# Kernel optimization log

Hardware: AMD Instinct MI355X
Metric: run time of the kernel (lower is better)

## Reference

```python
import jax, jax.numpy as jnp
import numpy as np

# dims: batch, d_features(m), n_subsets, sub_size(k=ceil(m/n)), heads, d_k, d_v, conv kernel, d_out
B, M, N, K, H, DK, DV, KER, D = 512, 4096, 64, 64, 8, 32, 4, 3, 4096
DOUT_PER = D // N  # d_out_per_subset = 64
EPS_LN = 1e-5      # torch nn.LayerNorm default eps


def setup_inputs() -> dict:
    key = jax.random.key(0)
    ks = jax.random.split(key, 8)
    s = 0.02  # xavier-like scale
    return {
        "features": jax.random.normal(ks[0], (B, M), dtype=jnp.float32),
        # per-head permutation of the m feature indices (f_shuffle(m, h, seeds))
        "shuffled_index": jnp.argsort(jax.random.uniform(ks[1], (H, M)), axis=1).astype(jnp.int32),
        "gamma": jnp.ones((M,), jnp.float32),
        "beta": jnp.zeros((M,), jnp.float32),
        "W_q": (jax.random.normal(ks[2], (H * DK, K)) * s).astype(jnp.float32),   # Linear(k, h*d_k)
        "W_k": (jax.random.normal(ks[3], (H, DK, K)) * s).astype(jnp.float32),    # grouped Conv1d(h, h*d_k, kernel=k, stride=k)
        "W_v1": (jax.random.normal(ks[4], (H, DV, KER)) * s).astype(jnp.float32), # grouped Conv1d(h, h*d_v, kernel)
        "W_v2": (jax.random.normal(ks[5], (H, DV)) * s).astype(jnp.float32),      # grouped Conv1d(h*d_v, h, 1)
        "W_fc": (jax.random.normal(ks[6], (DOUT_PER, H * K)) * s).astype(jnp.float32),
    }


def reference(features, shuffled_index, gamma, beta, W_q, W_k, W_v1, W_v2, W_fc):
    b = features.shape[0]
    # LayerNorm over m (query path only)
    mu = features.mean(-1, keepdims=True)
    var = ((features - mu) ** 2).mean(-1, keepdims=True)
    q_in = (features - mu) / jnp.sqrt(var + EPS_LN) * gamma + beta

    # shuffled gather: [b, H, M]  (k*n == m here so k_pad/q_pad are no-ops)
    sf = features[:, shuffled_index]

    # query: [b, n, k] -> Linear(k, h*d_k) -> [b, H, N, DK]
    q = jnp.einsum('bnk,ek->bne', q_in.reshape(b, N, K), W_q)
    q = q.reshape(b, N, H, DK).transpose(0, 2, 1, 3)

    # key: grouped conv kernel=stride=k == per-subset contraction -> [b, H, DK, N]
    kf = sf.reshape(b, H, N, K)
    key_ = jnp.einsum('bhnk,hdk->bhdn', kf, W_k)

    # value: [b, N, H, K], right-pad by KER-1, depthwise conv -> relu -> 1x1 conv -> +residual
    v = kf.transpose(0, 2, 1, 3)  # [b, N, H, K]
    vp = jnp.pad(v, ((0, 0), (0, 0), (0, 0), (0, KER - 1)))
    win = jnp.stack([vp[..., t:t + K] for t in range(KER)], axis=-1)  # [b,N,H,K,KER]
    v1 = jnp.einsum('bnhpt,hdt->bnhdp', win, W_v1)
    v2 = jnp.einsum('bnhdp,hd->bnhp', jax.nn.relu(v1), W_v2)
    v = (v2 + v).transpose(0, 2, 1, 3)  # [b, H, N, K]

    # scaled dot-product attention, temperature = sqrt(m)
    attn = jax.nn.softmax(jnp.einsum('bhqd,bhdk->bhqk', q, key_) / jnp.sqrt(jnp.float32(M)), axis=-1)
    out = jnp.einsum('bhqk,bhks->bhqs', attn, v)           # [b, H, N, K]
    out = out.transpose(0, 2, 1, 3).reshape(b, N, H * K)   # [b, N, H*K]
    out = jnp.einsum('bnf,of->bno', out, W_fc).reshape(b, N * DOUT_PER)
    return out, attn.reshape(b * H, N, N)
```

## Files before the change

### kernel.cpp

```cpp
#include <hip/hip_runtime.h>

typedef __bf16 v8bf __attribute__((ext_vector_type(8)));
typedef __bf16 v4bf __attribute__((ext_vector_type(4)));
typedef __bf16 v2bf __attribute__((ext_vector_type(2)));
typedef float  v4f  __attribute__((ext_vector_type(4)));
typedef float  v2f  __attribute__((ext_vector_type(2)));
typedef unsigned long long u64;

namespace {

constexpr int kB = 512, kM = 4096, kH = 8;


__global__ __launch_bounds__(256) void k0_weights(
    const float* __restrict__ Wq, const float* __restrict__ Wk,
    const float* __restrict__ Wfc,
    __bf16* __restrict__ wq, __bf16* __restrict__ wk, __bf16* __restrict__ wfc,
    float* __restrict__ out) {
  int i = blockIdx.x * 256 + threadIdx.x;
  float4 z = make_float4(0.f, 0.f, 0.f, 0.f);
#pragma unroll
  for (int j = 0; j < 4; ++j) reinterpret_cast<float4*>(out)[i + j * 131072] = z;
  if (i < 16384) {
    int e = i >> 6, k = i & 63;
    int dst = ((e >> 4) * 2 + (k >> 5)) * 512 + (e & 15) * 32 + (k & 31);
    wq[dst] = (__bf16)(Wq[i] * 0.015625f);
  } else if (i < 32768) {
    int j = i - 16384;
    int e = j >> 6, k = j & 63;
    int dst = ((e >> 4) * 2 + (k >> 5)) * 512 + (e & 15) * 32 + (k & 31);
    wk[dst] = (__bf16)Wk[j];
  } else if (i < 65536) {
    int j = i - 32768;
    int o = j >> 9, f = j & 511;
    int dst = ((o >> 4) * 16 + (f >> 5)) * 512 + (o & 15) * 32 + (f & 31);
    wfc[dst] = (__bf16)Wfc[j];
  }
}

__global__ __launch_bounds__(256, 4) void k_fused(
    const float* __restrict__ feat, const int* __restrict__ sidx,
    const float* __restrict__ gamma, const float* __restrict__ beta,
    const __bf16* __restrict__ wq, const __bf16* __restrict__ wk,
    const float* __restrict__ Wv1, const float* __restrict__ Wv2,
    const __bf16* __restrict__ wfc, float* __restrict__ out) {
  __shared__ __align__(16) __bf16 smem[19968];
  __shared__ float red[4];
  __bf16* s_feat = smem;
  __bf16* s_qin  = smem + 4096;
  __bf16* s_kf   = smem + 8192;
  __bf16* s_K    = smem + 12800;
  __bf16* s_vT   = smem + 15360;

  const int b = blockIdx.x, half = blockIdx.y, h0 = 4 * half;
  const int t = threadIdx.x, w = t >> 6, lane = t & 63;
  const int quad = lane >> 4, l16 = lane & 15;
  const int myrow = 16 * w + l16;

  const float4* frow4 = reinterpret_cast<const float4*>(feat + (size_t)b * kM);
  const float4* g4  = reinterpret_cast<const float4*>(gamma);
  const float4* be4 = reinterpret_cast<const float4*>(beta);
  float4 xs[4];
  float s = 0.f;
#pragma unroll
  for (int j = 0; j < 4; ++j) {
    xs[j] = frow4[t + j * 256];
    s += xs[j].x + xs[j].y + xs[j].z + xs[j].w;
  }
  int4 idxc[4], idxn[4];
  {
    const int* ibase = sidx + (size_t)h0 * kM + myrow * 64 + 8 * quad;
#pragma unroll
    for (int p = 0; p < 4; ++p)
      idxc[p] = *(const int4*)(ibase + 32 * (p >> 1) + 4 * (p & 1));
  }
#pragma unroll
  for (int o = 32; o > 0; o >>= 1) s += __shfl_xor(s, o);
  if (lane == 0) red[w] = s;
  __syncthreads();
  const float mu = (red[0] + red[1] + red[2] + red[3]) * (1.f / kM);
  float var_p = 0.f;
#pragma unroll
  for (int j = 0; j < 4; ++j) {
    float d0 = xs[j].x - mu, d1 = xs[j].y - mu, d2 = xs[j].z - mu, d3 = xs[j].w - mu;
    var_p += d0 * d0 + d1 * d1 + d2 * d2 + d3 * d3;
  }
#pragma unroll
  for (int o = 32; o > 0; o >>= 1) var_p += __shfl_xor(var_p, o);
  __syncthreads();
  if (lane == 0) red[w] = var_p;
  __syncthreads();
  const float var  = (red[0] + red[1] + red[2] + red[3]) * (1.f / kM);
  const float rstd = rsqrtf(var + 1e-5f);
#pragma unroll
  for (int j = 0; j < 4; ++j) {
    const int i4 = t + j * 256;
    float4 g = g4[i4], bt = be4[i4];
    v4bf fb, qb;
    fb[0] = (__bf16)xs[j].x; fb[1] = (__bf16)xs[j].y;
    fb[2] = (__bf16)xs[j].z; fb[3] = (__bf16)xs[j].w;
    qb[0] = (__bf16)((xs[j].x - mu) * rstd * g.x + bt.x);
    qb[1] = (__bf16)((xs[j].y - mu) * rstd * g.y + bt.y);
    qb[2] = (__bf16)((xs[j].z - mu) * rstd * g.z + bt.z);
    qb[3] = (__bf16)((xs[j].w - mu) * rstd * g.w + bt.w);
    *(v4bf*)(s_feat + 4 * i4) = fb;
    const int n = i4 >> 4, k = 4 * (t & 15);
    const int dst = ((n >> 4) * 2 + (k >> 5)) * 512 + (n & 15) * 32 + (k & 31);
    *(v4bf*)(s_qin + dst) = qb;
  }
  if (t < 64) { v8bf z = {}; *(v8bf*)(s_kf + t * 72 + 64) = z; }
  __syncthreads();

  v4f acc[4] = {{0.f, 0.f, 0.f, 0.f}, {0.f, 0.f, 0.f, 0.f},
                {0.f, 0.f, 0.f, 0.f}, {0.f, 0.f, 0.f, 0.f}};

  for (int it = 0; it < 4; ++it) {
    const int h = h0 + it;

    v8bf aq;
    {
      v4f dq0 = {0.f, 0.f, 0.f, 0.f}, dq1 = {0.f, 0.f, 0.f, 0.f};
#pragma unroll
      for (int kt = 0; kt < 2; ++kt) {
        v8bf a  = *(const v8bf*)(s_qin + (2 * w + kt) * 512 + l16 * 32 + 8 * quad);
        v8bf b0 = *(const v8bf*)(wq + (size_t)(4 * h + kt) * 512 + l16 * 32 + 8 * quad);
        v8bf b1 = *(const v8bf*)(wq + (size_t)(4 * h + 2 + kt) * 512 + l16 * 32 + 8 * quad);
        dq0 = __builtin_amdgcn_mfma_f32_16x16x32_bf16(b0, a, dq0, 0, 0, 0);
        dq1 = __builtin_amdgcn_mfma_f32_16x16x32_bf16(b1, a, dq1, 0, 0, 0);
      }
      v4bf p0, p1;
#pragma unroll
      for (int r = 0; r < 4; ++r) { p0[r] = (__bf16)dq0[r]; p1[r] = (__bf16)dq1[r]; }
      const u64 P0 = __builtin_bit_cast(u64, p0), P1 = __builtin_bit_cast(u64, p1);
      const int qs = 16 * (2 * (quad & 1));
      u64 s0p0 = __shfl(P0, l16 + qs),      s0p1 = __shfl(P1, l16 + qs);
      u64 s1p0 = __shfl(P0, l16 + qs + 16), s1p1 = __shfl(P1, l16 + qs + 16);
      v4bf lo = __builtin_bit_cast(v4bf, (quad >> 1) ? s0p1 : s0p0);
      v4bf hi = __builtin_bit_cast(v4bf, (quad >> 1) ? s1p1 : s1p0);
#pragma unroll
      for (int r = 0; r < 4; ++r) { aq[r] = lo[r]; aq[4 + r] = hi[r]; }
    }

    if (it < 3) {
      const int* ibase = sidx + (size_t)(h + 1) * kM + myrow * 64 + 8 * quad;
#pragma unroll
      for (int p = 0; p < 4; ++p)
        idxn[p] = *(const int4*)(ibase + 32 * (p >> 1) + 4 * (p & 1));
    }

    v8bf a0, a1;
    a0[0] = s_feat[idxc[0].x]; a0[1] = s_feat[idxc[0].y];
    a0[2] = s_feat[idxc[0].z]; a0[3] = s_feat[idxc[0].w];
    a0[4] = s_feat[idxc[1].x]; a0[5] = s_feat[idxc[1].y];
    a0[6] = s_feat[idxc[1].z]; a0[7] = s_feat[idxc[1].w];
    a1[0] = s_feat[idxc[2].x]; a1[1] = s_feat[idxc[2].y];
    a1[2] = s_feat[idxc[2].z]; a1[3] = s_feat[idxc[2].w];
    a1[4] = s_feat[idxc[3].x]; a1[5] = s_feat[idxc[3].y];
    a1[6] = s_feat[idxc[3].z]; a1[7] = s_feat[idxc[3].w];
    *(v8bf*)(s_kf + myrow * 72 + 8 * quad)      = a0;
    *(v8bf*)(s_kf + myrow * 72 + 32 + 8 * quad) = a1;

    {
      v4f dk0 = {0.f, 0.f, 0.f, 0.f}, dk1 = {0.f, 0.f, 0.f, 0.f};
      v8bf b00 = *(const v8bf*)(wk + (size_t)(4 * h + 0) * 512 + l16 * 32 + 8 * quad);
      v8bf b10 = *(const v8bf*)(wk + (size_t)(4 * h + 2) * 512 + l16 * 32 + 8 * quad);
      dk0 = __builtin_amdgcn_mfma_f32_16x16x32_bf16(b00, a0, dk0, 0, 0, 0);
      dk1 = __builtin_amdgcn_mfma_f32_16x16x32_bf16(b10, a0, dk1, 0, 0, 0);
      v8bf b01 = *(const v8bf*)(wk + (size_t)(4 * h + 1) * 512 + l16 * 32 + 8 * quad);
      v8bf b11 = *(const v8bf*)(wk + (size_t)(4 * h + 3) * 512 + l16 * 32 + 8 * quad);
      dk0 = __builtin_amdgcn_mfma_f32_16x16x32_bf16(b01, a1, dk0, 0, 0, 0);
      dk1 = __builtin_amdgcn_mfma_f32_16x16x32_bf16(b11, a1, dk1, 0, 0, 0);
      v4bf p0, p1;
#pragma unroll
      for (int r = 0; r < 4; ++r) { p0[r] = (__bf16)dk0[r]; p1[r] = (__bf16)dk1[r]; }
      *(v4bf*)(s_K + myrow * 40 + 4 * quad)      = p0;
      *(v4bf*)(s_K + myrow * 40 + 16 + 4 * quad) = p1;
    }
    __syncthreads();

    {
      const int n = lane, p0c = w * 16;
      float w1[4][3], w2[4];
#pragma unroll
      for (int d = 0; d < 4; ++d) {
#pragma unroll
        for (int c = 0; c < 3; ++c) w1[d][c] = Wv1[(h * 4 + d) * 3 + c];
        w2[d] = Wv2[h * 4 + d];
      }
      v8bf xa = *(const v8bf*)(s_kf + n * 72 + p0c);
      v8bf xb = *(const v8bf*)(s_kf + n * 72 + p0c + 8);
      v2bf xc = *(const v2bf*)(s_kf + n * 72 + p0c + 16);
      v2f x2[10];
#pragma unroll
      for (int j = 0; j < 8; ++j) { x2[j][0] = (float)xa[j]; x2[j][1] = (float)xb[j]; }
      x2[8][0] = (float)xb[0]; x2[8][1] = (float)xc[0];
      x2[9][0] = (float)xb[1]; x2[9][1] = (float)xc[1];
      const v2f z2 = {0.f, 0.f};
#pragma unroll
      for (int pp = 0; pp < 8; ++pp) {
        v2f a2 = x2[pp];
#pragma unroll
        for (int d = 0; d < 4; ++d) {
          v2f v1 = x2[pp] * w1[d][0] + x2[pp + 1] * w1[d][1] + x2[pp + 2] * w1[d][2];
          v1 = __builtin_elementwise_max(v1, z2);
          a2 = a2 + v1 * w2[d];
        }
        s_vT[(p0c + pp) * 72 + n]     = (__bf16)a2[0];
        s_vT[(p0c + pp + 8) * 72 + n] = (__bf16)a2[1];
      }
    }
    __syncthreads();

    v4f sc[4];
#pragma unroll
    for (int nt = 0; nt < 4; ++nt) {
      v4f zz = {0.f, 0.f, 0.f, 0.f};
      v8bf bbK = *(const v8bf*)(s_K + (16 * nt + l16) * 40 + 8 * quad);
      sc[nt] = __builtin_amdgcn_mfma_f32_16x16x32_bf16(bbK, aq, zz, 0, 0, 0);
    }

    float mx = sc[0][0];
#pragma unroll
    for (int nt = 0; nt < 4; ++nt)
#pragma unroll
      for (int r = 0; r < 4; ++r) mx = fmaxf(mx, sc[nt][r]);
    mx = fmaxf(mx, __shfl_xor(mx, 16));
    mx = fmaxf(mx, __shfl_xor(mx, 32));
    float ssum = 0.f;
#pragma unroll
    for (int nt = 0; nt < 4; ++nt)
#pragma unroll
      for (int r = 0; r < 4; ++r) {
        float e = __expf(sc[nt][r] - mx);
        sc[nt][r] = e; ssum += e;
      }
    ssum += __shfl_xor(ssum, 16);
    ssum += __shfl_xor(ssum, 32);
    const float inv = 1.0f / ssum;
#pragma unroll
    for (int nt = 0; nt < 4; ++nt) sc[nt] *= inv;

    float* attn_out = out + (size_t)kB * kM + ((size_t)(b * kH + h)) * 4096;
#pragma unroll
    for (int nt = 0; nt < 4; ++nt)
      *(v4f*)(attn_out + myrow * 64 + 16 * nt + 4 * quad) = sc[nt];

    v4bf P[4];
#pragma unroll
    for (int nt = 0; nt < 4; ++nt)
#pragma unroll
      for (int r = 0; r < 4; ++r) P[nt][r] = (__bf16)sc[nt][r];

    v4f dOT[4] = {{0.f, 0.f, 0.f, 0.f}, {0.f, 0.f, 0.f, 0.f},
                  {0.f, 0.f, 0.f, 0.f}, {0.f, 0.f, 0.f, 0.f}};
    const int src0 = l16 + 16 * (2 * (quad & 1));
#pragma unroll
    for (int kt = 0; kt < 2; ++kt) {
      const u64 pA = __builtin_bit_cast(u64, P[2 * kt]);
      const u64 pB = __builtin_bit_cast(u64, P[2 * kt + 1]);
      u64 A0 = __shfl(pA, src0), A1 = __shfl(pA, src0 + 16);
      u64 B0 = __shfl(pB, src0), B1 = __shfl(pB, src0 + 16);
      v4bf lo = __builtin_bit_cast(v4bf, (quad >> 1) ? B0 : A0);
      v4bf hi = __builtin_bit_cast(v4bf, (quad >> 1) ? B1 : A1);
      v8bf a_pv;
#pragma unroll
      for (int r = 0; r < 4; ++r) { a_pv[r] = lo[r]; a_pv[4 + r] = hi[r]; }
#pragma unroll
      for (int st = 0; st < 4; ++st) {
        v8bf bb = *(const v8bf*)(s_vT + (16 * st + l16) * 72 + 32 * kt + 8 * quad);
        dOT[st] = __builtin_amdgcn_mfma_f32_16x16x32_bf16(bb, a_pv, dOT[st], 0, 0, 0);
      }
    }
    __syncthreads();

    {
      v4bf Q[4];
#pragma unroll
      for (int st = 0; st < 4; ++st)
#pragma unroll
        for (int r = 0; r < 4; ++r) Q[st][r] = (__bf16)dOT[st][r];
#pragma unroll
      for (int kt = 0; kt < 2; ++kt) {
        const u64 qA = __builtin_bit_cast(u64, Q[2 * kt]);
        const u64 qB = __builtin_bit_cast(u64, Q[2 * kt + 1]);
        u64 A0 = __shfl(qA, src0), A1 = __shfl(qA, src0 + 16);
        u64 B0 = __shfl(qB, src0), B1 = __shfl(qB, src0 + 16);
        v4bf lo = __builtin_bit_cast(v4bf, (quad >> 1) ? B0 : A0);
        v4bf hi = __builtin_bit_cast(v4bf, (quad >> 1) ? B1 : A1);
        v8bf a_fc;
#pragma unroll
        for (int r = 0; r < 4; ++r) { a_fc[r] = lo[r]; a_fc[4 + r] = hi[r]; }
#pragma unroll
        for (int nt = 0; nt < 4; ++nt) {
          v8bf bb = *(const v8bf*)(wfc + (size_t)(nt * 16 + h * 2 + kt) * 512 + l16 * 32 + 8 * quad);
          acc[nt] = __builtin_amdgcn_mfma_f32_16x16x32_bf16(a_fc, bb, acc[nt], 0, 0, 0);
        }
      }
    }

    if (it < 3) {
#pragma unroll
      for (int p = 0; p < 4; ++p) idxc[p] = idxn[p];
    }
  }

  float* orow = out + (size_t)b * kM;
#pragma unroll
  for (int nt = 0; nt < 4; ++nt)
#pragma unroll
    for (int r = 0; r < 4; ++r)
      atomicAdd(&orow[(16 * w + 4 * quad + r) * 64 + 16 * nt + l16], acc[nt][r]);
}

}

extern "C" void kernel_launch(void* const* d_in, const int* in_sizes, int n_in,
                              void* d_out, int out_size, void* d_ws, size_t ws_size,
                              hipStream_t stream) {
  (void)in_sizes; (void)n_in; (void)out_size; (void)ws_size;
  const float* features = (const float*)d_in[0];
  const int*   sidx     = (const int*)d_in[1];
  const float* gamma    = (const float*)d_in[2];
  const float* beta     = (const float*)d_in[3];
  const float* Wq       = (const float*)d_in[4];
  const float* Wk       = (const float*)d_in[5];
  const float* Wv1      = (const float*)d_in[6];
  const float* Wv2      = (const float*)d_in[7];
  const float* Wfc      = (const float*)d_in[8];
  float* out = (float*)d_out;

  char* ws = (char*)d_ws;
  __bf16* ws_wq  = (__bf16*)(ws);
  __bf16* ws_wk  = (__bf16*)(ws + 32768);
  __bf16* ws_wfc = (__bf16*)(ws + 65536);

  hipLaunchKernelGGL(k0_weights, dim3(512), dim3(256), 0, stream,
                     Wq, Wk, Wfc, ws_wq, ws_wk, ws_wfc, out);
  hipLaunchKernelGGL(k_fused, dim3(kB, 2), dim3(256), 0, stream,
                     features, sidx, gamma, beta, ws_wq, ws_wk, Wv1, Wv2, ws_wfc, out);
}
```

Measured before the change: 135.9 us.

## Software-pipeline head loop: hoist Q projection, double-buffer K, defer FC

Computes all four heads' query projections up front, then aliases s_qin with s_kf to shrink shared memory. It double-buffers the key tile and defers each head's output FC MFMAs into the next iteration. The next head's gather is prefetched during the value conv phase, which removes one __syncthreads per head. The intent is to overlap independent work and cut barrier stalls, in exchange for more live registers (aq[4], Qprev, g0/g1) that may pressure occupancy at launch bounds of 4 blocks.

```diff
diff --git a/kernel.cpp b/kernel.cpp
--- a/kernel.cpp
+++ b/kernel.cpp
@@ -44,13 +44,14 @@
     const __bf16* __restrict__ wq, const __bf16* __restrict__ wk,
     const float* __restrict__ Wv1, const float* __restrict__ Wv2,
     const __bf16* __restrict__ wfc, float* __restrict__ out) {
-  __shared__ __align__(16) __bf16 smem[19968];
+  __shared__ __align__(16) __bf16 smem[18432];
   __shared__ float red[4];
   __bf16* s_feat = smem;
+  __bf16* s_kf   = smem + 4096;
+  __bf16* s_K0   = smem + 8704;
+  __bf16* s_K1   = smem + 11264;
+  __bf16* s_vT   = smem + 13824;
   __bf16* s_qin  = smem + 4096;
-  __bf16* s_kf   = smem + 8192;
-  __bf16* s_K    = smem + 12800;
-  __bf16* s_vT   = smem + 15360;
 
   const int b = blockIdx.x, half = blockIdx.y, h0 = 4 * half;
   const int t = threadIdx.x, w = t >> 6, lane = t & 63;
@@ -67,7 +68,7 @@
     xs[j] = frow4[t + j * 256];
     s += xs[j].x + xs[j].y + xs[j].z + xs[j].w;
   }
-  int4 idxc[4], idxn[4];
+  int4 idxc[4];
   {
     const int* ibase = sidx + (size_t)h0 * kM + myrow * 64 + 8 * quad;
 #pragma unroll
@@ -108,77 +109,108 @@
     const int dst = ((n >> 4) * 2 + (k >> 5)) * 512 + (n & 15) * 32 + (k & 31);
     *(v4bf*)(s_qin + dst) = qb;
   }
-  if (t < 64) { v8bf z = {}; *(v8bf*)(s_kf + t * 72 + 64) = z; }
-  __syncthreads();
-
-  v4f acc[4] = {{0.f, 0.f, 0.f, 0.f}, {0.f, 0.f, 0.f, 0.f},
-                {0.f, 0.f, 0.f, 0.f}, {0.f, 0.f, 0.f, 0.f}};
-
-  for (int it = 0; it < 4; ++it) {
-    const int h = h0 + it;
-
-    v8bf aq;
-    {
+  __syncthreads();
+
+  const int qs = 16 * (2 * (quad & 1));
+  v8bf aq[4];
+  {
+    v8bf aA0 = *(const v8bf*)(s_qin + (2 * w + 0) * 512 + l16 * 32 + 8 * quad);
+    v8bf aA1 = *(const v8bf*)(s_qin + (2 * w + 1) * 512 + l16 * 32 + 8 * quad);
+#pragma unroll
+    for (int itq = 0; itq < 4; ++itq) {
+      const int h = h0 + itq;
       v4f dq0 = {0.f, 0.f, 0.f, 0.f}, dq1 = {0.f, 0.f, 0.f, 0.f};
-#pragma unroll
-      for (int kt = 0; kt < 2; ++kt) {
-        v8bf a  = *(const v8bf*)(s_qin + (2 * w + kt) * 512 + l16 * 32 + 8 * quad);
-        v8bf b0 = *(const v8bf*)(wq + (size_t)(4 * h + kt) * 512 + l16 * 32 + 8 * quad);
-        v8bf b1 = *(const v8bf*)(wq + (size_t)(4 * h + 2 + kt) * 512 + l16 * 32 + 8 * quad);
-        dq0 = __builtin_amdgcn_mfma_f32_16x16x32_bf16(b0, a, dq0, 0, 0, 0);
-        dq1 = __builtin_amdgcn_mfma_f32_16x16x32_bf16(b1, a, dq1, 0, 0, 0);
-      }
+      v8bf b00 = *(const v8bf*)(wq + (size_t)(4 * h + 0) * 512 + l16 * 32 + 8 * quad);
+      v8bf b01 = *(const v8bf*)(wq + (size_t)(4 * h + 1) * 512 + l16 * 32 + 8 * quad);
+      v8bf b10 = *(const v8bf*)(wq + (size_t)(4 * h + 2) * 512 + l16 * 32 + 8 * quad);
+      v8bf b11 = *(const v8bf*)(wq + (size_t)(4 * h + 3) * 512 + l16 * 32 + 8 * quad);
+      dq0 = __builtin_amdgcn_mfma_f32_16x16x32_bf16(b00, aA0, dq0, 0, 0, 0);
+      dq0 = __builtin_amdgcn_mfma_f32_16x16x32_bf16(b01, aA1, dq0, 0, 0, 0);
+      dq1 = __builtin_amdgcn_mfma_f32_16x16x32_bf16(b10, aA0, dq1, 0, 0, 0);
+      dq1 = __builtin_amdgcn_mfma_f32_16x16x32_bf16(b11, aA1, dq1, 0, 0, 0);
       v4bf p0, p1;
 #pragma unroll
       for (int r = 0; r < 4; ++r) { p0[r] = (__bf16)dq0[r]; p1[r] = (__bf16)dq1[r]; }
       const u64 P0 = __builtin_bit_cast(u64, p0), P1 = __builtin_bit_cast(u64, p1);
-      const int qs = 16 * (2 * (quad & 1));
       u64 s0p0 = __shfl(P0, l16 + qs),      s0p1 = __shfl(P1, l16 + qs);
       u64 s1p0 = __shfl(P0, l16 + qs + 16), s1p1 = __shfl(P1, l16 + qs + 16);
       v4bf lo = __builtin_bit_cast(v4bf, (quad >> 1) ? s0p1 : s0p0);
       v4bf hi = __builtin_bit_cast(v4bf, (quad >> 1) ? s1p1 : s1p0);
 #pragma unroll
-      for (int r = 0; r < 4; ++r) { aq[r] = lo[r]; aq[4 + r] = hi[r]; }
-    }
-
-    if (it < 3) {
-      const int* ibase = sidx + (size_t)(h + 1) * kM + myrow * 64 + 8 * quad;
-#pragma unroll
-      for (int p = 0; p < 4; ++p)
-        idxn[p] = *(const int4*)(ibase + 32 * (p >> 1) + 4 * (p & 1));
-    }
-
-    v8bf a0, a1;
-    a0[0] = s_feat[idxc[0].x]; a0[1] = s_feat[idxc[0].y];
-    a0[2] = s_feat[idxc[0].z]; a0[3] = s_feat[idxc[0].w];
-    a0[4] = s_feat[idxc[1].x]; a0[5] = s_feat[idxc[1].y];
-    a0[6] = s_feat[idxc[1].z]; a0[7] = s_feat[idxc[1].w];
-    a1[0] = s_feat[idxc[2].x]; a1[1] = s_feat[idxc[2].y];
-    a1[2] = s_feat[idxc[2].z]; a1[3] = s_feat[idxc[2].w];
-    a1[4] = s_feat[idxc[3].x]; a1[5] = s_feat[idxc[3].y];
-    a1[6] = s_feat[idxc[3].z]; a1[7] = s_feat[idxc[3].w];
-    *(v8bf*)(s_kf + myrow * 72 + 8 * quad)      = a0;
-    *(v8bf*)(s_kf + myrow * 72 + 32 + 8 * quad) = a1;
-
+      for (int r = 0; r < 4; ++r) { aq[itq][r] = lo[r]; aq[itq][4 + r] = hi[r]; }
+    }
+  }
+
+  v8bf g0, g1;
+  g0[0] = s_feat[idxc[0].x]; g0[1] = s_feat[idxc[0].y];
+  g0[2] = s_feat[idxc[0].z]; g0[3] = s_feat[idxc[0].w];
+  g0[4] = s_feat[idxc[1].x]; g0[5] = s_feat[idxc[1].y];
+  g0[6] = s_feat[idxc[1].z]; g0[7] = s_feat[idxc[1].w];
+  g1[0] = s_feat[idxc[2].x]; g1[1] = s_feat[idxc[2].y];
+  g1[2] = s_feat[idxc[2].z]; g1[3] = s_feat[idxc[2].w];
+  g1[4] = s_feat[idxc[3].x]; g1[5] = s_feat[idxc[3].y];
+  g1[6] = s_feat[idxc[3].z]; g1[7] = s_feat[idxc[3].w];
+  __syncthreads();
+
+  if (t < 64) { v8bf z = {}; *(v8bf*)(s_kf + t * 72 + 64) = z; }
+
+  v4f acc[4] = {{0.f, 0.f, 0.f, 0.f}, {0.f, 0.f, 0.f, 0.f},
+                {0.f, 0.f, 0.f, 0.f}, {0.f, 0.f, 0.f, 0.f}};
+  v4bf Qprev[4];
+
+  for (int it = 0; it < 4; ++it) {
+    const int h = h0 + it;
+    __bf16* s_K = (it & 1) ? s_K1 : s_K0;
+
+    *(v8bf*)(s_kf + myrow * 72 + 8 * quad)      = g0;
+    *(v8bf*)(s_kf + myrow * 72 + 32 + 8 * quad) = g1;
     {
       v4f dk0 = {0.f, 0.f, 0.f, 0.f}, dk1 = {0.f, 0.f, 0.f, 0.f};
       v8bf b00 = *(const v8bf*)(wk + (size_t)(4 * h + 0) * 512 + l16 * 32 + 8 * quad);
       v8bf b10 = *(const v8bf*)(wk + (size_t)(4 * h + 2) * 512 + l16 * 32 + 8 * quad);
-      dk0 = __builtin_amdgcn_mfma_f32_16x16x32_bf16(b00, a0, dk0, 0, 0, 0);
-      dk1 = __builtin_amdgcn_mfma_f32_16x16x32_bf16(b10, a0, dk1, 0, 0, 0);
+      dk0 = __builtin_amdgcn_mfma_f32_16x16x32_bf16(b00, g0, dk0, 0, 0, 0);
+      dk1 = __builtin_amdgcn_mfma_f32_16x16x32_bf16(b10, g0, dk1, 0, 0, 0);
       v8bf b01 = *(const v8bf*)(wk + (size_t)(4 * h + 1) * 512 + l16 * 32 + 8 * quad);
       v8bf b11 = *(const v8bf*)(wk + (size_t)(4 * h + 3) * 512 + l16 * 32 + 8 * quad);
-      dk0 = __builtin_amdgcn_mfma_f32_16x16x32_bf16(b01, a1, dk0, 0, 0, 0);
-      dk1 = __builtin_amdgcn_mfma_f32_16x16x32_bf16(b11, a1, dk1, 0, 0, 0);
+      dk0 = __builtin_amdgcn_mfma_f32_16x16x32_bf16(b01, g1, dk0, 0, 0, 0);
+      dk1 = __builtin_amdgcn_mfma_f32_16x16x32_bf16(b11, g1, dk1, 0, 0, 0);
       v4bf p0, p1;
 #pragma unroll
       for (int r = 0; r < 4; ++r) { p0[r] = (__bf16)dk0[r]; p1[r] = (__bf16)dk1[r]; }
       *(v4bf*)(s_K + myrow * 40 + 4 * quad)      = p0;
       *(v4bf*)(s_K + myrow * 40 + 16 + 4 * quad) = p1;
     }
+
+    if (it > 0) {
+      const int hp = h - 1;
+#pragma unroll
+      for (int kt = 0; kt < 2; ++kt) {
+        const u64 qA = __builtin_bit_cast(u64, Qprev[2 * kt]);
+        const u64 qB = __builtin_bit_cast(u64, Qprev[2 * kt + 1]);
+        u64 A0 = __shfl(qA, l16 + qs), A1 = __shfl(qA, l16 + qs + 16);
+        u64 B0 = __shfl(qB, l16 + qs), B1 = __shfl(qB, l16 + qs + 16);
+        v4bf lo = __builtin_bit_cast(v4bf, (quad >> 1) ? B0 : A0);
+        v4bf hi = __builtin_bit_cast(v4bf, (quad >> 1) ? B1 : A1);
+        v8bf a_fc;
+#pragma unroll
+        for (int r = 0; r < 4; ++r) { a_fc[r] = lo[r]; a_fc[4 + r] = hi[r]; }
+#pragma unroll
+        for (int nt = 0; nt < 4; ++nt) {
+          v8bf bb = *(const v8bf*)(wfc + (size_t)(nt * 16 + hp * 2 + kt) * 512 + l16 * 32 + 8 * quad);
+          acc[nt] = __builtin_amdgcn_mfma_f32_16x16x32_bf16(a_fc, bb, acc[nt], 0, 0, 0);
+        }
+      }
+    }
     __syncthreads();
 
     {
+      int4 ixn[4];
+      if (it < 3) {
+        const int* ibase = sidx + (size_t)(h + 1) * kM + myrow * 64 + 8 * quad;
+#pragma unroll
+        for (int p = 0; p < 4; ++p)
+          ixn[p] = *(const int4*)(ibase + 32 * (p >> 1) + 4 * (p & 1));
+      }
       const int n = lane, p0c = w * 16;
       float w1[4][3], w2[4];
 #pragma unroll
@@ -208,6 +240,16 @@
         s_vT[(p0c + pp) * 72 + n]     = (__bf16)a2[0];
         s_vT[(p0c + pp + 8) * 72 + n] = (__bf16)a2[1];
       }
+      if (it < 3) {
+        g0[0] = s_feat[ixn[0].x]; g0[1] = s_feat[ixn[0].y];
+        g0[2] = s_feat[ixn[0].z]; g0[3] = s_feat[ixn[0].w];
+        g0[4] = s_feat[ixn[1].x]; g0[5] = s_feat[ixn[1].y];
+        g0[6] = s_feat[ixn[1].z]; g0[7] = s_feat[ixn[1].w];
+        g1[0] = s_feat[ixn[2].x]; g1[1] = s_feat[ixn[2].y];
+        g1[2] = s_feat[ixn[2].z]; g1[3] = s_feat[ixn[2].w];
+        g1[4] = s_feat[ixn[3].x]; g1[5] = s_feat[ixn[3].y];
+        g1[6] = s_feat[ixn[3].z]; g1[7] = s_feat[ixn[3].w];
+      }
     }
     __syncthreads();
 
@@ -216,7 +258,7 @@
     for (int nt = 0; nt < 4; ++nt) {
       v4f zz = {0.f, 0.f, 0.f, 0.f};
       v8bf bbK = *(const v8bf*)(s_K + (16 * nt + l16) * 40 + 8 * quad);
-      sc[nt] = __builtin_amdgcn_mfma_f32_16x16x32_bf16(bbK, aq, zz, 0, 0, 0);
+      sc[nt] = __builtin_amdgcn_mfma_f32_16x16x32_bf16(bbK, aq[it], zz, 0, 0, 0);
     }
 
     float mx = sc[0][0];
@@ -253,13 +295,12 @@
 
     v4f dOT[4] = {{0.f, 0.f, 0.f, 0.f}, {0.f, 0.f, 0.f, 0.f},
                   {0.f, 0.f, 0.f, 0.f}, {0.f, 0.f, 0.f, 0.f}};
-    const int src0 = l16 + 16 * (2 * (quad & 1));
 #pragma unroll
     for (int kt = 0; kt < 2; ++kt) {
       const u64 pA = __builtin_bit_cast(u64, P[2 * kt]);
       const u64 pB = __builtin_bit_cast(u64, P[2 * kt + 1]);
-      u64 A0 = __shfl(pA, src0), A1 = __shfl(pA, src0 + 16);
-      u64 B0 = __shfl(pB, src0), B1 = __shfl(pB, src0 + 16);
+      u64 A0 = __shfl(pA, l16 + qs), A1 = __shfl(pA, l16 + qs + 16);
+      u64 B0 = __shfl(pB, l16 + qs), B1 = __shfl(pB, l16 + qs + 16);
       v4bf lo = __builtin_bit_cast(v4bf, (quad >> 1) ? B0 : A0);
       v4bf hi = __builtin_bit_cast(v4bf, (quad >> 1) ? B1 : A1);
       v8bf a_pv;
@@ -271,36 +312,30 @@
         dOT[st] = __builtin_amdgcn_mfma_f32_16x16x32_bf16(bb, a_pv, dOT[st], 0, 0, 0);
       }
     }
-    __syncthreads();
-
-    {
-      v4bf Q[4];
-#pragma unroll
-      for (int st = 0; st < 4; ++st)
-#pragma unroll
-        for (int r = 0; r < 4; ++r) Q[st][r] = (__bf16)dOT[st][r];
-#pragma unroll
-      for (int kt = 0; kt < 2; ++kt) {
-        const u64 qA = __builtin_bit_cast(u64, Q[2 * kt]);
-        const u64 qB = __builtin_bit_cast(u64, Q[2 * kt + 1]);
-        u64 A0 = __shfl(qA, src0), A1 = __shfl(qA, src0 + 16);
-        u64 B0 = __shfl(qB, src0), B1 = __shfl(qB, src0 + 16);
-        v4bf lo = __builtin_bit_cast(v4bf, (quad >> 1) ? B0 : A0);
-        v4bf hi = __builtin_bit_cast(v4bf, (quad >> 1) ? B1 : A1);
-        v8bf a_fc;
-#pragma unroll
-        for (int r = 0; r < 4; ++r) { a_fc[r] = lo[r]; a_fc[4 + r] = hi[r]; }
-#pragma unroll
-        for (int nt = 0; nt < 4; ++nt) {
-          v8bf bb = *(const v8bf*)(wfc + (size_t)(nt * 16 + h * 2 + kt) * 512 + l16 * 32 + 8 * quad);
-          acc[nt] = __builtin_amdgcn_mfma_f32_16x16x32_bf16(a_fc, bb, acc[nt], 0, 0, 0);
-        }
-      }
-    }
-
-    if (it < 3) {
-#pragma unroll
-      for (int p = 0; p < 4; ++p) idxc[p] = idxn[p];
+#pragma unroll
+    for (int st = 0; st < 4; ++st)
+#pragma unroll
+      for (int r = 0; r < 4; ++r) Qprev[st][r] = (__bf16)dOT[st][r];
+  }
+
+  {
+    const int hp = h0 + 3;
+#pragma unroll
+    for (int kt = 0; kt < 2; ++kt) {
+      const u64 qA = __builtin_bit_cast(u64, Qprev[2 * kt]);
+      const u64 qB = __builtin_bit_cast(u64, Qprev[2 * kt + 1]);
+      u64 A0 = __shfl(qA, l16 + qs), A1 = __shfl(qA, l16 + qs + 16);
+      u64 B0 = __shfl(qB, l16 + qs), B1 = __shfl(qB, l16 + qs + 16);
+      v4bf lo = __builtin_bit_cast(v4bf, (quad >> 1) ? B0 : A0);
+      v4bf hi = __builtin_bit_cast(v4bf, (quad >> 1) ? B1 : A1);
+      v8bf a_fc;
+#pragma unroll
+      for (int r = 0; r < 4; ++r) { a_fc[r] = lo[r]; a_fc[4 + r] = hi[r]; }
+#pragma unroll
+      for (int nt = 0; nt < 4; ++nt) {
+        v8bf bb = *(const v8bf*)(wfc + (size_t)(nt * 16 + hp * 2 + kt) * 512 + l16 * 32 + 8 * quad);
+        acc[nt] = __builtin_amdgcn_mfma_f32_16x16x32_bf16(a_fc, bb, acc[nt], 0, 0, 0);
+      }
     }
   }
 
```

After: 130.9 us. 3.7% less time.
